# Kernel optimization log

Hardware: AMD Instinct MI355X
Metric: run time of the kernel (lower is better)

The kernel has to match this reference:

```python
import jax, jax.numpy as jnp
import numpy as np

K = 100
TEMPERATURE = 1.0


def setup_inputs() -> dict:
    key = jax.random.key(0)
    k1, k2, k3 = jax.random.split(key, 3)
    student_emb = jax.random.normal(k1, (8, 512, 1500), dtype=jnp.float32)
    teacher_codes = jax.random.randint(k2, (8, 1500), 0, 4096, dtype=jnp.int64)
    codebook = jax.random.normal(k3, (4096, 512), dtype=jnp.float32)
    return {"student_emb": student_emb, "teacher_codes": teacher_codes, "codebook": codebook}


def reference(student_emb, teacher_codes, codebook):
    B, C, T = student_emb.shape
    # flatten tokens: (N, C) with N = B*T
    emb = jnp.transpose(student_emb, (0, 2, 1)).reshape(-1, C)
    codes = teacher_codes.reshape(-1).astype(jnp.int32)

    # Euclidean cdist via the ||a||^2 + ||b||^2 - 2ab expansion (same math as torch.cdist)
    emb_sq = jnp.sum(emb * emb, axis=1, keepdims=True)            # (N,1)
    cb_sq = jnp.sum(codebook * codebook, axis=1)[None, :]         # (1,V)
    d2 = emb_sq + cb_sq - 2.0 * jnp.matmul(emb, codebook.T)       # (N,V)
    distances = jnp.sqrt(jnp.maximum(d2, 0.0))

    # top-k smallest distances
    _, top_k_indices = jax.lax.top_k(-distances, K)               # (N,K)

    # include_correct: replace last candidate with the true code if absent
    correct_in_topk = jnp.any(top_k_indices == codes[:, None], axis=1)
    top_k_indices = top_k_indices.at[:, -1].set(
        jnp.where(correct_in_topk, top_k_indices[:, -1], codes))

    candidate_distances = jnp.take_along_axis(distances, top_k_indices, axis=1)
    logits = -candidate_distances / TEMPERATURE                   # (N,K)

    match = top_k_indices == codes[:, None]
    local_labels = jnp.argmax(match.astype(jnp.int32), axis=1)    # (N,)

    logp = jax.nn.log_softmax(logits, axis=1)
    loss = -jnp.mean(jnp.take_along_axis(logp, local_labels[:, None], axis=1))

    local_predictions = jnp.argmax(logits, axis=-1)
    local_accuracy = jnp.mean((local_predictions == local_labels).astype(jnp.float32))
    global_predictions = jnp.argmin(distances, axis=-1)
    global_accuracy = jnp.mean((global_predictions == codes).astype(jnp.float32))
    correct_in_candidates = jnp.mean(jnp.any(top_k_indices == codes[:, None], axis=1).astype(jnp.float32))

    return loss, local_accuracy, global_accuracy, correct_in_candidates
```

## Files before the change

kernel.cpp:

```cpp
#include <hip/hip_runtime.h>
#include <hip/hip_bf16.h>
#include <cstdint>

#define B_ 8
#define C_ 512
#define T_ 1500
#define N_ (B_*T_)
#define NPAD_ 12032
#define V_ 4096
#define K_ 100

typedef unsigned long long u64;
typedef __attribute__((ext_vector_type(8))) short short8;
typedef __attribute__((ext_vector_type(8))) unsigned short u16x8;
typedef __attribute__((ext_vector_type(4))) float f32x4;

__device__ __forceinline__ unsigned short f2bf(float x){
    __hip_bfloat16 h = __float2bfloat16(x);
    return __builtin_bit_cast(unsigned short, h);
}
__device__ __forceinline__ unsigned short f2h(float x){
    return __builtin_bit_cast(unsigned short, (_Float16)x);
}
__device__ __forceinline__ float h2f(unsigned short h){
    return (float)__builtin_bit_cast(_Float16, h);
}

__device__ __forceinline__ void gll16(const unsigned short* g, unsigned short* l){
    __builtin_amdgcn_global_load_lds(
        (const __attribute__((address_space(1))) void*)g,
        (__attribute__((address_space(3))) void*)l, 16, 0, 0);
}

__global__ __launch_bounds__(256) void cbconv_kernel(const float* __restrict__ CB,
                                                     unsigned short* __restrict__ CBh,
                                                     float* __restrict__ csq){
    int wv = threadIdx.x >> 6, lane = threadIdx.x & 63;
    int r = blockIdx.x * 4 + wv;
    const float4* p4 = (const float4*)(CB + (size_t)r * C_);
    ushort4* o4 = (ushort4*)(CBh + (size_t)r * C_);
    float s = 0.f;
    #pragma unroll
    for (int j = 0; j < 2; ++j){
        float4 v = p4[lane + j*64];
        s += v.x*v.x + v.y*v.y + v.z*v.z + v.w*v.w;
        ushort4 h; h.x = f2bf(v.x); h.y = f2bf(v.y); h.z = f2bf(v.z); h.w = f2bf(v.w);
        o4[lane + j*64] = h;
    }
    #pragma unroll
    for (int o = 32; o; o >>= 1) s += __shfl_down(s, o, 64);
    if (lane == 0) csq[r] = s;
}

__global__ __launch_bounds__(256) void transpose_conv_kernel(const float* __restrict__ S,
                                                             unsigned short* __restrict__ embT,
                                                             float* __restrict__ esq){
    __shared__ float tile[32][33];
    __shared__ float psum[8][33];
    int b  = blockIdx.z;
    int c0 = blockIdx.y * 32;
    int t0 = blockIdx.x * 32;
    int tx = threadIdx.x, ty = threadIdx.y;
    #pragma unroll
    for (int r = 0; r < 4; ++r){
        int c = c0 + ty + r*8;
        int t = t0 + tx;
        tile[ty + r*8][tx] = (t < T_) ? S[((size_t)b*C_ + c)*T_ + t] : 0.f;
    }
    __syncthreads();
    float ps = 0.f;
    #pragma unroll
    for (int r = 0; r < 4; ++r){ float v = tile[ty + r*8][tx]; ps += v * v; }
    psum[ty][tx] = ps;
    #pragma unroll
    for (int r = 0; r < 4; ++r){
        int t = t0 + ty + r*8;
        int c = c0 + tx;
        if (t < T_) embT[((size_t)b*T_ + t)*C_ + c] = f2bf(tile[tx][ty + r*8]);
    }
    __syncthreads();
    if (ty == 0){
        int t = t0 + tx;
        if (t < T_){
            float s2 = 0.f;
            #pragma unroll
            for (int w = 0; w < 8; ++w) s2 += psum[w][tx];
            atomicAdd(&esq[b*T_ + t], s2);
        }
    }
}

__global__ __launch_bounds__(256) void gemm_dot_kernel(
    const unsigned short* __restrict__ A, const unsigned short* __restrict__ Bm,
    unsigned short* __restrict__ doth, int row_lo, int row_hi)
{
    __shared__ unsigned short As[128*32];
    __shared__ unsigned short Bs[128*32];
    int tid = threadIdx.x, lane = tid & 63, wv = tid >> 6;
    int row0 = row_lo + blockIdx.x * 128;
    int col0 = blockIdx.y * 128;

    int sr = lane >> 2;
    int sk = (lane & 3) * 8;
    int ar0 = row0 + wv*32 + sr;       int ar1 = ar0 + 16;
    int ca0 = (ar0 < N_) ? ar0 : N_-1; int ca1 = (ar1 < N_) ? ar1 : N_-1;
    const unsigned short* Ap0 = A  + (size_t)ca0 * C_ + sk;
    const unsigned short* Ap1 = A  + (size_t)ca1 * C_ + sk;
    const unsigned short* Bp0 = Bm + (size_t)(col0 + wv*32 + sr) * C_ + sk;
    const unsigned short* Bp1 = Bp0 + (size_t)16 * C_;
    unsigned short* Ad0 = &As[(wv*32     ) * 32];
    unsigned short* Ad1 = &As[(wv*32 + 16) * 32];
    unsigned short* Bd0 = &Bs[(wv*32     ) * 32];
    unsigned short* Bd1 = &Bs[(wv*32 + 16) * 32];

    int wm = (wv >> 1) * 64, wn = (wv & 1) * 64;
    int fr = lane & 15;
    int fk = (lane >> 4) * 8;

    f32x4 acc[4][4];
    #pragma unroll
    for (int i = 0; i < 4; ++i)
        #pragma unroll
        for (int j = 0; j < 4; ++j) acc[i][j] = (f32x4){0.f, 0.f, 0.f, 0.f};

    for (int kt = 0; kt < C_/32; ++kt){
        int k0 = kt * 32;
        gll16(Ap0 + k0, Ad0);
        gll16(Ap1 + k0, Ad1);
        gll16(Bp0 + k0, Bd0);
        gll16(Bp1 + k0, Bd1);
        __syncthreads();
        short8 af[4], bf[4];
        #pragma unroll
        for (int i = 0; i < 4; ++i) af[i] = *(const short8*)&As[(wm + i*16 + fr)*32 + fk];
        #pragma unroll
        for (int j = 0; j < 4; ++j) bf[j] = *(const short8*)&Bs[(wn + j*16 + fr)*32 + fk];
        #pragma unroll
        for (int i = 0; i < 4; ++i)
            #pragma unroll
            for (int j = 0; j < 4; ++j)
                acc[i][j] = __builtin_amdgcn_mfma_f32_16x16x32_bf16(af[i], bf[j], acc[i][j], 0, 0, 0);
        __syncthreads();
    }

    int er = (lane >> 4) * 4;
    int ec = lane & 15;
    #pragma unroll
    for (int i = 0; i < 4; ++i){
        #pragma unroll
        for (int r = 0; r < 4; ++r){
            int n = row0 + wm + i*16 + er + r;
            if (n >= row_hi) continue;
            size_t base = (size_t)(n - row_lo) * V_;
            #pragma unroll
            for (int j = 0; j < 4; ++j){
                int v = col0 + wn + j*16 + ec;
                doth[base + v] = f2h(acc[i][j][r]);
            }
        }
    }
}

__global__ __launch_bounds__(256, 2) void select_kernel(const unsigned short* __restrict__ doth,
                                                        const int* __restrict__ codes,
                                                        const float* __restrict__ esq,
                                                        const float* __restrict__ csq,
                                                        float2* __restrict__ pairbuf,
                                                        int row_lo, int nrows){
    int tid = threadIdx.x, lane = tid & 63, wv = tid >> 6;
    int lrow = blockIdx.x * 4 + wv;
    if (lrow >= nrows) return;
    int n = row_lo + lrow;
    const u16x8* r8 = (const u16x8*)(doth + (size_t)lrow * V_);

    __shared__ unsigned hist[4][256] __attribute__((aligned(16)));
    __shared__ unsigned coll[4][64];
    __shared__ unsigned collcnt[4];

    float esq_n = esq[n];
    int code = codes[n];
    float dotc = h2f(doth[(size_t)lrow * V_ + code]);
    unsigned ucode = __float_as_uint(fmaxf(esq_n + csq[code] - 2.f * dotc, 0.f));

    unsigned u[64];
    #pragma unroll
    for (int j = 0; j < 8; ++j){
        u16x8 h = r8[lane + j*64];
        const float4* cp = (const float4*)(csq + 8*lane + 512*j);
        float4 c0 = cp[0], c1 = cp[1];
        float cs[8] = {c0.x, c0.y, c0.z, c0.w, c1.x, c1.y, c1.z, c1.w};
        #pragma unroll
        for (int e = 0; e < 8; ++e){
            float d2 = fmaxf(esq_n + cs[e] - 2.f * h2f(h[e]), 0.f);
            u[8*j+e] = __float_as_uint(d2);
        }
    }

    unsigned umin = u[0], umax = u[0];
    #pragma unroll
    for (int k = 1; k < 64; ++k){
        umin = (u[k] < umin) ? u[k] : umin;
        umax = (u[k] > umax) ? u[k] : umax;
    }
    #pragma unroll
    for (int o = 32; o; o >>= 1){
        unsigned a = (unsigned)__shfl_xor((int)umin, o, 64); if (a < umin) umin = a;
        unsigned b = (unsigned)__shfl_xor((int)umax, o, 64); if (b > umax) umax = b;
    }
    unsigned im = 0xFFFFFFFFu;
    #pragma unroll
    for (int k = 0; k < 64; ++k){
        unsigned idx = 8u*(unsigned)lane + (unsigned)(512*(k >> 3) + (k & 7));
        if (u[k] == umin && idx < im) im = idx;
    }
    #pragma unroll
    for (int o = 32; o; o >>= 1){
        unsigned a = (unsigned)__shfl_xor((int)im, o, 64); if (a < im) im = a;
    }
    int idx0 = (int)im;
    float d0 = sqrtf(__uint_as_float(umin));

    unsigned t;
    if (umin == umax){
        t = umin;
    } else {
        ((uint4*)&hist[wv][0])[lane] = (uint4){0u,0u,0u,0u};
        if (lane == 0) collcnt[wv] = 0u;
        asm volatile("s_waitcnt lgkmcnt(0)" ::: "memory");
        float fmn = __uint_as_float(umin), fmx = __uint_as_float(umax);
        float invw = 256.0f / (fmx - fmn);
        #pragma unroll
        for (int k = 0; k < 64; ++k){
            float fk = __uint_as_float(u[k]);
            int b = (int)((fk - fmn) * invw); b = (b > 255) ? 255 : b;
            atomicAdd(&hist[wv][b], 1u);
        }
        asm volatile("s_waitcnt lgkmcnt(0)" ::: "memory");
        uint4 hq = ((uint4*)&hist[wv][0])[lane];
        unsigned lsum = hq.x + hq.y + hq.z + hq.w;
        unsigned inc = lsum;
        #pragma unroll
        for (int o = 1; o < 64; o <<= 1){
            unsigned y = (unsigned)__shfl_up((int)inc, o, 64);
            if (lane >= o) inc += y;
        }
        unsigned e0 = inc - lsum;
        unsigned e1 = e0 + hq.x, e2 = e1 + hq.y, e3 = e2 + hq.z, e4 = e3 + hq.w;
        int sel = -1;
        if      (e0 <= 99u && 99u < e1) sel = 0;
        else if (e1 <= 99u && 99u < e2) sel = 1;
        else if (e2 <= 99u && 99u < e3) sel = 2;
        else if (e3 <= 99u && 99u < e4) sel = 3;
        u64 bal = __ballot(sel >= 0);
        int src = __ffsll(bal) - 1;
        unsigned myBk = (unsigned)(4*lane + (sel < 0 ? 0 : sel));
        unsigned myBase = (sel == 1) ? e1 : (sel == 2) ? e2 : (sel == 3) ? e3 : e0;
        int Bk   = __shfl((int)myBk,   src, 64);
        int base = __shfl((int)myBase, src, 64);
        int rk = 99 - base;
        #pragma unroll
        for (int k = 0; k < 64; ++k){
            float fk = __uint_as_float(u[k]);
            int b = (int)((fk - fmn) * invw); b = (b > 255) ? 255 : b;
            if (b == Bk){
                unsigned pos = atomicAdd(&collcnt[wv], 1u);
                if (pos < 64u) coll[wv][pos] = u[k];
            }
        }
        asm volatile("s_waitcnt lgkmcnt(0)" ::: "memory");
        unsigned bcnt = collcnt[wv];
        if (bcnt <= 64u){
            unsigned w = (lane < (int)bcnt) ? coll[wv][lane] : 0xFFFFFFFFu;
            unsigned wmn = (lane < (int)bcnt) ? w : 0xFFFFFFFFu;
            unsigned wmx = (lane < (int)bcnt) ? w : 0u;
            #pragma unroll
            for (int o = 32; o; o >>= 1){
                unsigned a = (unsigned)__shfl_xor((int)wmn, o, 64); if (a < wmn) wmn = a;
                unsigned b = (unsigned)__shfl_xor((int)wmx, o, 64); if (b > wmx) wmx = b;
            }
            unsigned P;
            if (wmn == wmx) P = wmn;
            else {
                int hb = 31 - __clz((int)(wmn ^ wmx));
                unsigned mask = (hb == 31) ? 0xFFFFFFFFu : ((1u << (hb+1)) - 1u);
                P = wmn & ~mask;
                for (int b = hb; b >= 0; --b){
                    unsigned cand = P | (1u << b);
                    int c = __popcll(__ballot(w < cand));
                    if (c <= rk) P = cand;
                }
            }
            t = P;
        } else {
            int hb = 31 - __clz((int)(umin ^ umax));
            unsigned mask = (hb == 31) ? 0xFFFFFFFFu : ((1u << (hb+1)) - 1u);
            unsigned P = umin & ~mask;
            for (int b = hb; b >= 0; --b){
                unsigned cand = P | (1u << b);
                int c = 0;
                #pragma unroll
                for (int k = 0; k < 64; ++k) c += (u[k] < cand) ? 1 : 0;
                #pragma unroll
                for (int o = 32; o; o >>= 1) c += __shfl_xor(c, o, 64);
                if (c <= 99) P = cand;
            }
            t = P;
        }
    }
    float tval = sqrtf(__uint_as_float(t));

    float s = 0.f; int cl = 0;
    #pragma unroll
    for (int k = 0; k < 64; ++k){
        if (u[k] < t){ s += __expf(d0 - sqrtf(__uint_as_float(u[k]))); cl++; }
    }
    #pragma unroll
    for (int o = 32; o; o >>= 1){
        s += __shfl_xor(s, o, 64);
        cl += __shfl_xor(cl, o, 64);
    }
    if (lane == 0){
        float S = s + (float)(K_ - cl) * __expf(d0 - tval);
        float dcode = sqrtf(__uint_as_float(ucode));
        if (ucode > t) S += __expf(d0 - dcode) - __expf(d0 - tval);
        float nll = dcode - d0 + __logf(S);
        pairbuf[n] = make_float2(nll, (idx0 == code) ? 1.f : 0.f);
    }
}

__global__ __launch_bounds__(1024) void finalize_kernel(const float2* __restrict__ pair,
                                                        float* __restrict__ out){
    int tid = threadIdx.x;
    float sn = 0.f, sh = 0.f;
    for (int i = tid; i < N_; i += 1024){
        float2 p = pair[i]; sn += p.x; sh += p.y;
    }
    #pragma unroll
    for (int o = 32; o; o >>= 1){ sn += __shfl_down(sn, o, 64); sh += __shfl_down(sh, o, 64); }
    __shared__ float a[16], b[16];
    int wv = tid >> 6, lane = tid & 63;
    if (lane == 0){ a[wv] = sn; b[wv] = sh; }
    __syncthreads();
    if (tid == 0){
        float L = 0.f, H = 0.f;
        #pragma unroll
        for (int i = 0; i < 16; ++i){ L += a[i]; H += b[i]; }
        out[0] = L / (float)N_;
        out[1] = H / (float)N_;
        out[2] = H / (float)N_;
        out[3] = 1.0f;
    }
}

extern "C" void kernel_launch(void* const* d_in, const int* in_sizes, int n_in,
                              void* d_out, int out_size, void* d_ws, size_t ws_size,
                              hipStream_t stream){
    const float* S   = (const float*)d_in[0];
    const int* codes = (const int*)d_in[1];
    const float* CB  = (const float*)d_in[2];
    float* out = (float*)d_out;

    char* w = (char*)d_ws;
    size_t off = 0;
    unsigned short* embT = (unsigned short*)(w + off); off += (size_t)NPAD_ * C_ * 2;
    unsigned short* CBh  = (unsigned short*)(w + off); off += (size_t)V_ * C_ * 2;
    float* csq = (float*)(w + off); off += (size_t)V_ * 4;
    float* esq = (float*)(w + off); off += (size_t)N_ * 4;
    off = (off + 255) & ~(size_t)255;
    float2* pairbuf = (float2*)(w + off); off += (size_t)N_ * 8;
    unsigned short* dotbuf = (unsigned short*)(w + off);

    size_t avail = (ws_size > off) ? ws_size - off : 0;
    long maxrows = (long)(avail / ((size_t)V_ * 2));
    int chunk = (maxrows >= N_) ? N_ : (int)maxrows;
    if (chunk < 4) chunk = 4;

    hipMemsetAsync(esq, 0, (size_t)N_ * 4, stream);
    hipLaunchKernelGGL(cbconv_kernel, dim3(V_/4), dim3(256), 0, stream, CB, CBh, csq);
    hipLaunchKernelGGL(transpose_conv_kernel, dim3((T_+31)/32, C_/32, B_), dim3(32, 8), 0, stream,
                       S, embT, esq);

    for (int row_lo = 0; row_lo < N_; row_lo += chunk){
        int row_hi = row_lo + chunk; if (row_hi > N_) row_hi = N_;
        int rows = row_hi - row_lo;
        hipLaunchKernelGGL(gemm_dot_kernel, dim3((rows + 127)/128, V_/128), dim3(256), 0, stream,
                           embT, CBh, dotbuf, row_lo, row_hi);
        hipLaunchKernelGGL(select_kernel, dim3((rows + 3)/4), dim3(256), 0, stream,
                           dotbuf, codes, esq, csq, pairbuf, row_lo, rows);
    }
    hipLaunchKernelGGL(finalize_kernel, dim3(1), dim3(1024), 0, stream, pairbuf, out);
}
```

Before: 221.1 us.

## Triple-buffer GEMM LDS loads and vectorize fp16 output stores

The bf16 MFMA GEMM now uses three LDS stages with direct global-to-LDS loads issued two K-steps ahead. Partial vmcnt waits and a single barrier per step replace the two syncthreads, so memory latency overlaps compute. The MFMA operands are swapped so each lane holds four consecutive columns, letting the epilogue write 8-byte ushort4 stores instead of scalar 2-byte stores. This triples shared memory use per block, which may reduce occupancy.

After: 229.6 us. 1.04x slower.

```diff
diff --git a/kernel.cpp b/kernel.cpp
--- a/kernel.cpp
+++ b/kernel.cpp
@@ -94,8 +94,8 @@
     const unsigned short* __restrict__ A, const unsigned short* __restrict__ Bm,
     unsigned short* __restrict__ doth, int row_lo, int row_hi)
 {
-    __shared__ unsigned short As[128*32];
-    __shared__ unsigned short Bs[128*32];
+    __shared__ unsigned short As[3][128*32];
+    __shared__ unsigned short Bs[3][128*32];
     int tid = threadIdx.x, lane = tid & 63, wv = tid >> 6;
     int row0 = row_lo + blockIdx.x * 128;
     int col0 = blockIdx.y * 128;
@@ -108,10 +108,6 @@
     const unsigned short* Ap1 = A  + (size_t)ca1 * C_ + sk;
     const unsigned short* Bp0 = Bm + (size_t)(col0 + wv*32 + sr) * C_ + sk;
     const unsigned short* Bp1 = Bp0 + (size_t)16 * C_;
-    unsigned short* Ad0 = &As[(wv*32     ) * 32];
-    unsigned short* Ad1 = &As[(wv*32 + 16) * 32];
-    unsigned short* Bd0 = &Bs[(wv*32     ) * 32];
-    unsigned short* Bd1 = &Bs[(wv*32 + 16) * 32];
 
     int wm = (wv >> 1) * 64, wn = (wv & 1) * 64;
     int fr = lane & 15;
@@ -123,40 +119,62 @@
         #pragma unroll
         for (int j = 0; j < 4; ++j) acc[i][j] = (f32x4){0.f, 0.f, 0.f, 0.f};
 
-    for (int kt = 0; kt < C_/32; ++kt){
+    auto stage = [&](int s, int kt){
         int k0 = kt * 32;
-        gll16(Ap0 + k0, Ad0);
-        gll16(Ap1 + k0, Ad1);
-        gll16(Bp0 + k0, Bd0);
-        gll16(Bp1 + k0, Bd1);
-        __syncthreads();
+        gll16(Ap0 + k0, &As[s][(wv*32     ) * 32]);
+        gll16(Ap1 + k0, &As[s][(wv*32 + 16) * 32]);
+        gll16(Bp0 + k0, &Bs[s][(wv*32     ) * 32]);
+        gll16(Bp1 + k0, &Bs[s][(wv*32 + 16) * 32]);
+    };
+    auto compute = [&](int s){
         short8 af[4], bf[4];
         #pragma unroll
-        for (int i = 0; i < 4; ++i) af[i] = *(const short8*)&As[(wm + i*16 + fr)*32 + fk];
-        #pragma unroll
-        for (int j = 0; j < 4; ++j) bf[j] = *(const short8*)&Bs[(wn + j*16 + fr)*32 + fk];
+        for (int i = 0; i < 4; ++i) af[i] = *(const short8*)&As[s][(wm + i*16 + fr)*32 + fk];
+        #pragma unroll
+        for (int j = 0; j < 4; ++j) bf[j] = *(const short8*)&Bs[s][(wn + j*16 + fr)*32 + fk];
         #pragma unroll
         for (int i = 0; i < 4; ++i)
             #pragma unroll
             for (int j = 0; j < 4; ++j)
-                acc[i][j] = __builtin_amdgcn_mfma_f32_16x16x32_bf16(af[i], bf[j], acc[i][j], 0, 0, 0);
-        __syncthreads();
-    }
-
-    int er = (lane >> 4) * 4;
-    int ec = lane & 15;
+                acc[i][j] = __builtin_amdgcn_mfma_f32_16x16x32_bf16(bf[j], af[i], acc[i][j], 0, 0, 0);
+    };
+
+    stage(0, 0);
+    stage(1, 1);
+
+    #pragma unroll
+    for (int kt = 0; kt < 14; ++kt){
+        asm volatile("s_waitcnt vmcnt(4)" ::: "memory");
+        __builtin_amdgcn_s_barrier();
+        asm volatile("" ::: "memory");
+        stage((kt + 2) % 3, kt + 2);
+        compute(kt % 3);
+    }
+    asm volatile("s_waitcnt vmcnt(4)" ::: "memory");
+    __builtin_amdgcn_s_barrier();
+    asm volatile("" ::: "memory");
+    compute(14 % 3);
+    asm volatile("s_waitcnt vmcnt(0)" ::: "memory");
+    __builtin_amdgcn_s_barrier();
+    asm volatile("" ::: "memory");
+    compute(15 % 3);
+
+    int en = lane & 15;
+    int ev = (lane >> 4) * 4;
     #pragma unroll
     for (int i = 0; i < 4; ++i){
-        #pragma unroll
-        for (int r = 0; r < 4; ++r){
-            int n = row0 + wm + i*16 + er + r;
-            if (n >= row_hi) continue;
-            size_t base = (size_t)(n - row_lo) * V_;
-            #pragma unroll
-            for (int j = 0; j < 4; ++j){
-                int v = col0 + wn + j*16 + ec;
-                doth[base + v] = f2h(acc[i][j][r]);
-            }
+        int n = row0 + wm + i*16 + en;
+        if (n >= row_hi) continue;
+        size_t base = (size_t)(n - row_lo) * V_;
+        int vb = col0 + wn + ev;
+        #pragma unroll
+        for (int j = 0; j < 4; ++j){
+            ushort4 h;
+            h.x = f2h(acc[i][j][0]);
+            h.y = f2h(acc[i][j][1]);
+            h.z = f2h(acc[i][j][2]);
+            h.w = f2h(acc[i][j][3]);
+            *(ushort4*)&doth[base + vb + j*16] = h;
         }
     }
 }
```
